# Optimization experiments

Hardware: AMD Instinct MI355X
Metric: run time of the kernel (lower is better)

Reference implementation:

```python
import jax, jax.numpy as jnp
import numpy as np

N, E, D_IN, HEADS, C = 100000, 1600000, 128, 4, 32  # C = out_channels per head


def setup_inputs() -> dict:
    key = jax.random.key(0)
    ks = jax.random.split(key, 10)
    s = 1.0 / np.sqrt(D_IN)
    return {
        "x": jax.random.normal(ks[0], (N, D_IN), jnp.float32),
        "edge_index": jax.random.randint(ks[1], (2, E), 0, N, jnp.int64),
        "Wq": jax.random.normal(ks[2], (D_IN, HEADS * C), jnp.float32) * s,
        "bq": jnp.zeros((HEADS * C,), jnp.float32),
        "Wk": jax.random.normal(ks[3], (D_IN, HEADS * C), jnp.float32) * s,
        "bk": jnp.zeros((HEADS * C,), jnp.float32),
        "Wv": jax.random.normal(ks[4], (D_IN, HEADS * C), jnp.float32) * s,
        "bv": jnp.zeros((HEADS * C,), jnp.float32),
        "Wskip": jax.random.normal(ks[5], (D_IN, HEADS * C), jnp.float32) * s,
        "bskip": jnp.zeros((HEADS * C,), jnp.float32),
    }


def reference(x, edge_index, Wq, bq, Wk, bk, Wv, bv, Wskip, bskip):
    n = x.shape[0]
    src, dst = edge_index[0], edge_index[1]  # message flows src (j) -> dst (i)
    q = (x @ Wq + bq).reshape(n, HEADS, C)
    k = (x @ Wk + bk).reshape(n, HEADS, C)
    v = (x @ Wv + bv).reshape(n, HEADS, C)

    # per-edge attention logits [E, H]
    alpha = jnp.einsum('ehc,ehc->eh', q[dst], k[src]) / jnp.sqrt(jnp.float32(C))

    # segment softmax over incoming edges of each target node
    m = jax.ops.segment_max(alpha, dst, num_segments=n)          # [N, H]
    p = jnp.exp(alpha - m[dst])                                   # [E, H]
    z = jax.ops.segment_sum(p, dst, num_segments=n)               # [N, H]
    w = p / (z[dst] + 1e-16)                                      # [E, H]

    # softmax-weighted scatter aggregation of values
    out = jax.ops.segment_sum(v[src] * w[:, :, None], dst, num_segments=n)
    out = out.reshape(n, HEADS * C)

    # root/skip connection (beta=False default: plain add)
    out = out + x @ Wskip + bskip
    return out
```

## Files before the change

### kernel.cpp

```cpp
#include <hip/hip_runtime.h>

#define DIN 128
#define NHEADS 4
#define CH 32
#define MT 128
#define CHUNK 4096
#define NPB 256
#define EPB_IT 25

typedef _Float16 h8 __attribute__((ext_vector_type(8)));
typedef float f4 __attribute__((ext_vector_type(4)));

__global__ __launch_bounds__(256) void cvt_x(
    const float* __restrict__ x, _Float16* __restrict__ xh, int n4)
{
    int i = blockIdx.x * 256 + threadIdx.x;
    if (i >= n4) return;
    float4 xv = reinterpret_cast<const float4*>(x)[i];
    _Float16 h[4] = {(_Float16)xv.x, (_Float16)xv.y, (_Float16)xv.z, (_Float16)xv.w};
    reinterpret_cast<uint2*>(xh)[i] = *reinterpret_cast<uint2*>(h);
}

__global__ __launch_bounds__(256) void prep_w(
    const float* __restrict__ Wq, const float* __restrict__ Wk,
    const float* __restrict__ Wv, const float* __restrict__ Wsk,
    _Float16* __restrict__ wt)
{
    int i = blockIdx.x * 256 + threadIdx.x;
    if (i >= 4 * 16384) return;
    int mat = i >> 14;
    int rem = i & 16383;
    int n  = rem >> 7;
    int kk = rem & 127;
    const float* W = (mat == 0) ? Wq : (mat == 1) ? Wk : (mat == 2) ? Wv : Wsk;
    wt[i] = (_Float16)W[kk * 128 + n];
}

__global__ __launch_bounds__(256) void qkvs_mfma(
    const _Float16* __restrict__ xh, const _Float16* __restrict__ wt,
    const float* __restrict__ bq, const float* __restrict__ bk,
    const float* __restrict__ bv, const float* __restrict__ bsk,
    _Float16* __restrict__ qh, _Float16* __restrict__ kvh,
    float* __restrict__ outskip, int N)
{
    __shared__ _Float16 As[MT * 128];
    const int t = threadIdx.x;
    const int rowBase = blockIdx.x * MT;
    const int mat = blockIdx.y;

    for (int i = t; i < MT * 16; i += 256) {
        int r  = i >> 4;
        int c8 = i & 15;
        uint4 val = make_uint4(0u, 0u, 0u, 0u);
        int gr = rowBase + r;
        if (gr < N)
            val = reinterpret_cast<const uint4*>(xh)[(size_t)gr * 16 + c8];
        *reinterpret_cast<uint4*>(&As[r * 128 + ((c8 ^ (r & 7)) << 3)]) = val;
    }
    __syncthreads();

    const int wid  = t >> 6;
    const int l    = t & 63;
    const int lm   = l & 15;
    const int quad = l >> 4;

    const _Float16* __restrict__ Bsrc = wt + (size_t)mat * 16384;

    f4 acc[2][8];
    #pragma unroll
    for (int ms = 0; ms < 2; ++ms)
        #pragma unroll
        for (int nt = 0; nt < 8; ++nt)
            acc[ms][nt] = (f4){0.f, 0.f, 0.f, 0.f};

    #pragma unroll
    for (int kq = 0; kq < 4; ++kq) {
        const int c8 = kq * 4 + quad;
        const int k0 = c8 << 3;
        h8 a0 = *reinterpret_cast<const h8*>(
            &As[(wid * 32 + lm) * 128 + ((c8 ^ (lm & 7)) << 3)]);
        h8 a1 = *reinterpret_cast<const h8*>(
            &As[(wid * 32 + 16 + lm) * 128 + ((c8 ^ (lm & 7)) << 3)]);
        #pragma unroll
        for (int nt = 0; nt < 8; ++nt) {
            h8 b = *reinterpret_cast<const h8*>(
                &Bsrc[(size_t)(nt * 16 + lm) * 128 + k0]);
            acc[0][nt] = __builtin_amdgcn_mfma_f32_16x16x32_f16(a0, b, acc[0][nt], 0, 0, 0);
            acc[1][nt] = __builtin_amdgcn_mfma_f32_16x16x32_f16(a1, b, acc[1][nt], 0, 0, 0);
        }
    }

    const float* bias = (mat == 0) ? bq : (mat == 1) ? bk : (mat == 2) ? bv : bsk;

    #pragma unroll
    for (int ms = 0; ms < 2; ++ms) {
        #pragma unroll
        for (int nt = 0; nt < 8; ++nt) {
            int col = nt * 16 + lm;
            float bsv = bias[col];
            #pragma unroll
            for (int i2 = 0; i2 < 4; ++i2) {
                int row = rowBase + wid * 32 + ms * 16 + quad * 4 + i2;
                if (row < N) {
                    float val = acc[ms][nt][i2] + bsv;
                    if (mat == 3)
                        outskip[(size_t)row * 128 + col] = val;
                    else if (mat == 0)
                        qh[(size_t)row * 128 + col] = (_Float16)val;
                    else {
                        size_t off = (size_t)row * 256 + ((col >> 2) << 3)
                                   + (col & 3) + ((mat == 2) ? 4 : 0);
                        kvh[off] = (_Float16)val;
                    }
                }
            }
        }
    }
}

__global__ __launch_bounds__(256) void bucket_hist(
    const int* __restrict__ ei, int* __restrict__ bcnt, int E, int nb)
{
    __shared__ int lds[512];
    for (int b = threadIdx.x; b < nb; b += 256) lds[b] = 0;
    __syncthreads();
    for (long long i = (long long)blockIdx.x * 256 + threadIdx.x; i < E;
         i += (long long)gridDim.x * 256)
        atomicAdd(&lds[ei[(size_t)E + i] >> 8], 1);
    __syncthreads();
    for (int b = threadIdx.x; b < nb; b += 256)
        if (lds[b]) atomicAdd(&bcnt[b], lds[b]);
}

__global__ __launch_bounds__(512) void scan_buckets(
    const int* __restrict__ bcnt, int* __restrict__ boff,
    int* __restrict__ bcur, int nb)
{
    __shared__ int ws[8];
    int t = threadIdx.x, lane = t & 63, wid = t >> 6;
    int v = (t < nb) ? bcnt[t] : 0;
    int s = v;
    #pragma unroll
    for (int off = 1; off < 64; off <<= 1) {
        int n = __shfl_up(s, off);
        if (lane >= off) s += n;
    }
    if (lane == 63) ws[wid] = s;
    __syncthreads();
    int add = 0;
    for (int w = 0; w < wid; ++w) add += ws[w];
    int excl = s - v + add;
    if (t < nb) { boff[t] = excl; bcur[t] = excl; }
    if (t == nb - 1) boff[nb] = excl + v;
}

__global__ __launch_bounds__(256) void bucket_scatter(
    const int* __restrict__ ei, int* __restrict__ bcur,
    uint2* __restrict__ pairs, int E, int nb)
{
    __shared__ int cnt[512];
    int t = threadIdx.x;
    for (int b = t; b < nb; b += 256) cnt[b] = 0;
    __syncthreads();

    long long e0 = (long long)blockIdx.x * (256 * EPB_IT);
    int ps[EPB_IT], pd[EPB_IT];
    #pragma unroll
    for (int j = 0; j < EPB_IT; ++j) {
        long long e = e0 + j * 256 + t;
        if (e < E) {
            ps[j] = ei[e];
            pd[j] = ei[(size_t)E + e];
            atomicAdd(&cnt[pd[j] >> 8], 1);
        } else pd[j] = -1;
    }
    __syncthreads();
    for (int b = t; b < nb; b += 256) {
        int c = cnt[b];
        if (c) cnt[b] = atomicAdd(&bcur[b], c);
    }
    __syncthreads();
    #pragma unroll
    for (int j = 0; j < EPB_IT; ++j) {
        if (pd[j] >= 0) {
            int pos = atomicAdd(&cnt[pd[j] >> 8], 1);
            pairs[pos] = make_uint2((unsigned)ps[j], (unsigned)pd[j]);
        }
    }
}

__global__ __launch_bounds__(256) void bucket_counts(
    const uint2* __restrict__ pairs, const int* __restrict__ boff,
    int* __restrict__ counts, int N)
{
    __shared__ int cnt[NPB];
    int b = blockIdx.x, t = threadIdx.x;
    cnt[t] = 0;
    __syncthreads();
    int s = boff[b], e = boff[b + 1];
    for (int i = s + t; i < e; i += 256)
        atomicAdd(&cnt[pairs[i].y & (NPB - 1)], 1);
    __syncthreads();
    int node = b * NPB + t;
    if (node < N) counts[node] = cnt[t];
}

__global__ __launch_bounds__(256) void chunk_sums(
    const int* __restrict__ counts, int* __restrict__ partials, int N)
{
    int b = blockIdx.x, t = threadIdx.x;
    int base = b * CHUNK + t * 16;
    int s = 0;
    #pragma unroll
    for (int j = 0; j < 16; ++j) {
        int i = base + j;
        if (i < N) s += counts[i];
    }
    #pragma unroll
    for (int off = 1; off < 64; off <<= 1) s += __shfl_xor(s, off);
    __shared__ int ws[4];
    int lane = t & 63, wid = t >> 6;
    if (lane == 0) ws[wid] = s;
    __syncthreads();
    if (t == 0) partials[b] = ws[0] + ws[1] + ws[2] + ws[3];
}

__global__ __launch_bounds__(256) void scan_chunks(
    const int* __restrict__ partials, int* __restrict__ chunkoff, int nch)
{
    __shared__ int ws[4];
    int t = threadIdx.x, lane = t & 63, wid = t >> 6;
    int v = (t < nch) ? partials[t] : 0;
    int s = v;
    #pragma unroll
    for (int off = 1; off < 64; off <<= 1) {
        int n = __shfl_up(s, off);
        if (lane >= off) s += n;
    }
    if (lane == 63) ws[wid] = s;
    __syncthreads();
    int add = 0;
    for (int w = 0; w < wid; ++w) add += ws[w];
    if (t < nch) chunkoff[t] = s - v + add;
}

__global__ __launch_bounds__(256) void scan_write(
    const int* __restrict__ counts, const int* __restrict__ chunkoff,
    int* __restrict__ rowptr, int N)
{
    int b = blockIdx.x, t = threadIdx.x;
    int base = b * CHUNK + t * 16;
    int vals[16];
    int s = 0;
    #pragma unroll
    for (int j = 0; j < 16; ++j) {
        int i = base + j;
        vals[j] = (i < N) ? counts[i] : 0;
        s += vals[j];
    }
    int lane = t & 63, wid = t >> 6;
    int incl = s;
    #pragma unroll
    for (int off = 1; off < 64; off <<= 1) {
        int n = __shfl_up(incl, off);
        if (lane >= off) incl += n;
    }
    __shared__ int ws[4];
    if (lane == 63) ws[wid] = incl;
    __syncthreads();
    int add = chunkoff[b];
    for (int w = 0; w < wid; ++w) add += ws[w];
    int run = incl - s + add;
    #pragma unroll
    for (int j = 0; j < 16; ++j) {
        int i = base + j;
        if (i < N) rowptr[i + 1] = run + vals[j];
        run += vals[j];
    }
    if (b == 0 && t == 0) rowptr[0] = 0;
}

__global__ __launch_bounds__(256) void bucket_place(
    const uint2* __restrict__ pairs, const int* __restrict__ boff,
    const int* __restrict__ rowptr, int* __restrict__ sorted, int N)
{
    __shared__ int cur[NPB];
    int b = blockIdx.x, t = threadIdx.x;
    int node = b * NPB + t;
    cur[t] = (node < N) ? rowptr[node] : 0;
    __syncthreads();
    int s = boff[b], e = boff[b + 1];
    for (int i = s + t; i < e; i += 256) {
        uint2 pr = pairs[i];
        int pos = atomicAdd(&cur[pr.y & (NPB - 1)], 1);
        sorted[pos] = (int)pr.x;
    }
}

__device__ inline float4 cvt4(uint2 r) {
    union { uint2 u; _Float16 h[4]; } c;
    c.u = r;
    return make_float4((float)c.h[0], (float)c.h[1], (float)c.h[2], (float)c.h[3]);
}

__global__ __launch_bounds__(256) void node_aggregate(
    const _Float16* __restrict__ q, const _Float16* __restrict__ kv,
    const int* __restrict__ rowptr, const int* __restrict__ srcs,
    float* __restrict__ out, int N)
{
    int gid  = blockIdx.x * 256 + threadIdx.x;
    int node = gid >> 5;
    if (node >= N) return;
    int l = gid & 31;

    float4 qv = cvt4(reinterpret_cast<const uint2*>(q + (size_t)node * 128)[l]);
    float4 acc = make_float4(0.f, 0.f, 0.f, 0.f);
    float z = 0.f;

    const uint4* kv4 = reinterpret_cast<const uint4*>(kv);
    const float SC = 0.17677669529663687f;
    int e0 = rowptr[node], e1 = rowptr[node + 1];
    int e = e0;
    for (; e + 4 <= e1; e += 4) {
        int s0 = srcs[e], s1 = srcs[e + 1], s2 = srcs[e + 2], s3 = srcs[e + 3];
        uint4 r0 = kv4[(size_t)s0 * 32 + l];
        uint4 r1 = kv4[(size_t)s1 * 32 + l];
        uint4 r2 = kv4[(size_t)s2 * 32 + l];
        uint4 r3 = kv4[(size_t)s3 * 32 + l];
        float4 k0 = cvt4(make_uint2(r0.x, r0.y)), v0 = cvt4(make_uint2(r0.z, r0.w));
        float4 k1 = cvt4(make_uint2(r1.x, r1.y)), v1 = cvt4(make_uint2(r1.z, r1.w));
        float4 k2 = cvt4(make_uint2(r2.x, r2.y)), v2 = cvt4(make_uint2(r2.z, r2.w));
        float4 k3 = cvt4(make_uint2(r3.x, r3.y)), v3 = cvt4(make_uint2(r3.z, r3.w));
        float sa = qv.x * k0.x + qv.y * k0.y + qv.z * k0.z + qv.w * k0.w;
        float sb = qv.x * k1.x + qv.y * k1.y + qv.z * k1.z + qv.w * k1.w;
        float sc = qv.x * k2.x + qv.y * k2.y + qv.z * k2.z + qv.w * k2.w;
        float sd = qv.x * k3.x + qv.y * k3.y + qv.z * k3.z + qv.w * k3.w;
        sa += __shfl_xor(sa, 1); sb += __shfl_xor(sb, 1);
        sc += __shfl_xor(sc, 1); sd += __shfl_xor(sd, 1);
        sa += __shfl_xor(sa, 2); sb += __shfl_xor(sb, 2);
        sc += __shfl_xor(sc, 2); sd += __shfl_xor(sd, 2);
        sa += __shfl_xor(sa, 4); sb += __shfl_xor(sb, 4);
        sc += __shfl_xor(sc, 4); sd += __shfl_xor(sd, 4);
        float pa = __expf(sa * SC), pb = __expf(sb * SC);
        float pc = __expf(sc * SC), pdd = __expf(sd * SC);
        z += (pa + pb) + (pc + pdd);
        acc.x += pa * v0.x + pb * v1.x + pc * v2.x + pdd * v3.x;
        acc.y += pa * v0.y + pb * v1.y + pc * v2.y + pdd * v3.y;
        acc.z += pa * v0.z + pb * v1.z + pc * v2.z + pdd * v3.z;
        acc.w += pa * v0.w + pb * v1.w + pc * v2.w + pdd * v3.w;
    }
    for (; e < e1; ++e) {
        int s0 = srcs[e];
        uint4 r0 = kv4[(size_t)s0 * 32 + l];
        float4 k0 = cvt4(make_uint2(r0.x, r0.y)), v0 = cvt4(make_uint2(r0.z, r0.w));
        float sa = qv.x * k0.x + qv.y * k0.y + qv.z * k0.z + qv.w * k0.w;
        sa += __shfl_xor(sa, 1);
        sa += __shfl_xor(sa, 2);
        sa += __shfl_xor(sa, 4);
        float pa = __expf(sa * SC);
        z += pa;
        acc.x += pa * v0.x; acc.y += pa * v0.y;
        acc.z += pa * v0.z; acc.w += pa * v0.w;
    }

    float inv = 1.f / (z + 1e-16f);
    float4 o = reinterpret_cast<float4*>(out)[(size_t)node * 32 + l];
    o.x += acc.x * inv; o.y += acc.y * inv;
    o.z += acc.z * inv; o.w += acc.w * inv;
    reinterpret_cast<float4*>(out)[(size_t)node * 32 + l] = o;
}

extern "C" void kernel_launch(void* const* d_in, const int* in_sizes, int n_in,
                              void* d_out, int out_size, void* d_ws, size_t ws_size,
                              hipStream_t stream)
{
    const float* x   = (const float*)d_in[0];
    const int*   ei  = (const int*)d_in[1];
    const float* Wq  = (const float*)d_in[2];
    const float* bq  = (const float*)d_in[3];
    const float* Wk  = (const float*)d_in[4];
    const float* bk  = (const float*)d_in[5];
    const float* Wv  = (const float*)d_in[6];
    const float* bv  = (const float*)d_in[7];
    const float* Wsk = (const float*)d_in[8];
    const float* bsk = (const float*)d_in[9];
    float* out = (float*)d_out;

    const int N = in_sizes[0] / DIN;
    const int E = in_sizes[1] / 2;
    const int nb = (N + NPB - 1) / NPB;

    _Float16* xh  = (_Float16*)d_ws;
    _Float16* qh  = xh + (size_t)N * DIN;
    _Float16* kvh = qh + (size_t)N * DIN;
    _Float16* wt  = kvh + (size_t)N * 256;
    uint2* pairs  = (uint2*)(wt + 4 * 16384);
    int* sorted   = (int*)(pairs + (size_t)E);
    int* counts   = sorted + E;
    int* rowptr   = counts + N;
    int* bcnt     = rowptr + (N + 1);
    int* boff     = bcnt + 512;
    int* bcur     = boff + 513;
    int* partials = bcur + 512;
    int* chunkoff = partials + 256;

    hipMemsetAsync(bcnt, 0, 512 * sizeof(int), stream);

    int n4 = N * DIN / 4;
    cvt_x<<<(n4 + 255) / 256, 256, 0, stream>>>(x, xh, n4);
    prep_w<<<(4 * 16384 + 255) / 256, 256, 0, stream>>>(Wq, Wk, Wv, Wsk, wt);

    dim3 ggrid((N + MT - 1) / MT, 4);
    qkvs_mfma<<<ggrid, 256, 0, stream>>>(xh, wt, bq, bk, bv, bsk,
                                         qh, kvh, out, N);

    bucket_hist<<<256, 256, 0, stream>>>(ei, bcnt, E, nb);
    scan_buckets<<<1, 512, 0, stream>>>(bcnt, boff, bcur, nb);
    int sb = (E + 256 * EPB_IT - 1) / (256 * EPB_IT);
    bucket_scatter<<<sb, 256, 0, stream>>>(ei, bcur, pairs, E, nb);
    bucket_counts<<<nb, 256, 0, stream>>>(pairs, boff, counts, N);

    int nch = (N + CHUNK - 1) / CHUNK;
    chunk_sums<<<nch, 256, 0, stream>>>(counts, partials, N);
    scan_chunks<<<1, 256, 0, stream>>>(partials, chunkoff, nch);
    scan_write<<<nch, 256, 0, stream>>>(counts, chunkoff, rowptr, N);

    bucket_place<<<nb, 256, 0, stream>>>(pairs, boff, rowptr, sorted, N);

    int ab = (N * 32 + 255) / 256;
    node_aggregate<<<ab, 256, 0, stream>>>(qh, kvh, rowptr, sorted, out, N);
}
```

Before: 438.3 us.

## Fuse CSR build into persistent grid-synced kernel and convert x inside GEMM

Replaces the chain of small CSR-construction kernels (histogram, scans, scatter, counts, place) plus weight prep with a single persistent 512-block kernel that uses atomic-counter grid barriers between phases. The QKV/skip GEMM now reads fp32 x directly and converts to fp16 while staging into LDS, so the separate conversion kernel and its fp16 copy of x are gone. Each block also loops over all four weight matrices instead of using a 4-wide grid. This removes many launch gaps and one full pass over x, at the cost of spin-wait barriers that only work if all 512 blocks are co-resident, and less GEMM parallelism per launch.

```diff
diff --git a/kernel.cpp b/kernel.cpp
--- a/kernel.cpp
+++ b/kernel.cpp
@@ -7,37 +7,202 @@
 #define CHUNK 4096
 #define NPB 256
 #define EPB_IT 25
+#define CSR_GRID 512
 
 typedef _Float16 h8 __attribute__((ext_vector_type(8)));
 typedef float f4 __attribute__((ext_vector_type(4)));
 
-__global__ __launch_bounds__(256) void cvt_x(
-    const float* __restrict__ x, _Float16* __restrict__ xh, int n4)
-{
-    int i = blockIdx.x * 256 + threadIdx.x;
-    if (i >= n4) return;
-    float4 xv = reinterpret_cast<const float4*>(x)[i];
-    _Float16 h[4] = {(_Float16)xv.x, (_Float16)xv.y, (_Float16)xv.z, (_Float16)xv.w};
-    reinterpret_cast<uint2*>(xh)[i] = *reinterpret_cast<uint2*>(h);
-}
-
-__global__ __launch_bounds__(256) void prep_w(
+__device__ __forceinline__ void gsync(int* bar, int idx, int nblk) {
+    __syncthreads();
+    if (threadIdx.x == 0) {
+        __threadfence();
+        atomicAdd(&bar[idx], 1);
+        while (atomicAdd(&bar[idx], 0) < nblk)
+            __builtin_amdgcn_s_sleep(2);
+    }
+    __syncthreads();
+    __threadfence();
+}
+
+__global__ __launch_bounds__(256, 4) void coop_csr(
     const float* __restrict__ Wq, const float* __restrict__ Wk,
     const float* __restrict__ Wv, const float* __restrict__ Wsk,
-    _Float16* __restrict__ wt)
+    _Float16* __restrict__ wt,
+    const int* __restrict__ ei, uint2* __restrict__ pairs,
+    int* __restrict__ sorted, int* __restrict__ counts,
+    int* __restrict__ rowptr, int* __restrict__ bar, int* __restrict__ bcnt,
+    int* __restrict__ boff, int* __restrict__ bcur,
+    int* __restrict__ partials, int* __restrict__ chunkoff,
+    int E, int N, int nb, int nch)
 {
-    int i = blockIdx.x * 256 + threadIdx.x;
-    if (i >= 4 * 16384) return;
-    int mat = i >> 14;
-    int rem = i & 16383;
-    int n  = rem >> 7;
-    int kk = rem & 127;
-    const float* W = (mat == 0) ? Wq : (mat == 1) ? Wk : (mat == 2) ? Wv : Wsk;
-    wt[i] = (_Float16)W[kk * 128 + n];
+    __shared__ int smem[512];
+    __shared__ int ws[8];
+    const int b = blockIdx.x, t = threadIdx.x;
+    const int nblk = gridDim.x;
+
+    for (int i = b * 256 + t; i < 4 * 16384; i += nblk * 256) {
+        int mat = i >> 14;
+        int rem = i & 16383;
+        int n  = rem >> 7;
+        int kk = rem & 127;
+        const float* W = (mat == 0) ? Wq : (mat == 1) ? Wk : (mat == 2) ? Wv : Wsk;
+        wt[i] = (_Float16)W[kk * 128 + n];
+    }
+    gsync(bar, 0, nblk);
+
+    for (int i = t; i < nb; i += 256) smem[i] = 0;
+    __syncthreads();
+    for (long long i = (long long)b * 256 + t; i < E; i += (long long)nblk * 256)
+        atomicAdd(&smem[ei[(size_t)E + i] >> 8], 1);
+    __syncthreads();
+    for (int i = t; i < nb; i += 256)
+        if (smem[i]) atomicAdd(&bcnt[i], smem[i]);
+    gsync(bar, 1, nblk);
+
+    if (b == 0) {
+        int i0 = 2 * t, i1 = 2 * t + 1;
+        int a = (i0 < nb) ? bcnt[i0] : 0;
+        int c = (i1 < nb) ? bcnt[i1] : 0;
+        int s = a + c;
+        int lane = t & 63, wid = t >> 6;
+        int incl = s;
+        #pragma unroll
+        for (int off = 1; off < 64; off <<= 1) {
+            int n = __shfl_up(incl, off);
+            if (lane >= off) incl += n;
+        }
+        if (lane == 63) ws[wid] = incl;
+        __syncthreads();
+        int add = 0;
+        for (int w = 0; w < wid; ++w) add += ws[w];
+        int excl = incl - s + add;
+        if (i0 < nb) { boff[i0] = excl;     bcur[i0] = excl; }
+        if (i1 < nb) { boff[i1] = excl + a; bcur[i1] = excl + a; }
+        if (t == 255) boff[nb] = excl + s;
+    }
+    gsync(bar, 2, nblk);
+
+    for (long long c0 = (long long)b * (256 * EPB_IT); c0 < E;
+         c0 += (long long)nblk * (256 * EPB_IT)) {
+        for (int i = t; i < nb; i += 256) smem[i] = 0;
+        __syncthreads();
+        int ps[EPB_IT], pd[EPB_IT];
+        #pragma unroll
+        for (int j = 0; j < EPB_IT; ++j) {
+            long long e = c0 + j * 256 + t;
+            if (e < E) {
+                ps[j] = ei[e];
+                pd[j] = ei[(size_t)E + e];
+                atomicAdd(&smem[pd[j] >> 8], 1);
+            } else pd[j] = -1;
+        }
+        __syncthreads();
+        for (int i = t; i < nb; i += 256) {
+            int c = smem[i];
+            if (c) smem[i] = atomicAdd(&bcur[i], c);
+        }
+        __syncthreads();
+        #pragma unroll
+        for (int j = 0; j < EPB_IT; ++j) {
+            if (pd[j] >= 0) {
+                int pos = atomicAdd(&smem[pd[j] >> 8], 1);
+                pairs[pos] = make_uint2((unsigned)ps[j], (unsigned)pd[j]);
+            }
+        }
+        __syncthreads();
+    }
+    gsync(bar, 3, nblk);
+
+    for (int bb = b; bb < nb; bb += nblk) {
+        smem[t] = 0;
+        __syncthreads();
+        int s = boff[bb], e = boff[bb + 1];
+        for (int i = s + t; i < e; i += 256)
+            atomicAdd(&smem[pairs[i].y & (NPB - 1)], 1);
+        __syncthreads();
+        int node = bb * NPB + t;
+        if (node < N) counts[node] = smem[t];
+        __syncthreads();
+    }
+    gsync(bar, 4, nblk);
+
+    if (b < nch) {
+        int base = b * CHUNK + t * 16;
+        int s = 0;
+        #pragma unroll
+        for (int j = 0; j < 16; ++j) {
+            int i = base + j;
+            if (i < N) s += counts[i];
+        }
+        #pragma unroll
+        for (int off = 1; off < 64; off <<= 1) s += __shfl_xor(s, off);
+        int lane = t & 63, wid = t >> 6;
+        if (lane == 0) ws[wid] = s;
+        __syncthreads();
+        if (t == 0) partials[b] = ws[0] + ws[1] + ws[2] + ws[3];
+    }
+    gsync(bar, 5, nblk);
+
+    if (b == 0 && t < 64) {
+        int v = (t < nch) ? partials[t] : 0;
+        int s = v;
+        #pragma unroll
+        for (int off = 1; off < 64; off <<= 1) {
+            int n = __shfl_up(s, off);
+            if (t >= off) s += n;
+        }
+        if (t < nch) chunkoff[t] = s - v;
+    }
+    gsync(bar, 6, nblk);
+
+    if (b < nch) {
+        int base = b * CHUNK + t * 16;
+        int vals[16];
+        int s = 0;
+        #pragma unroll
+        for (int j = 0; j < 16; ++j) {
+            int i = base + j;
+            vals[j] = (i < N) ? counts[i] : 0;
+            s += vals[j];
+        }
+        int lane = t & 63, wid = t >> 6;
+        int incl = s;
+        #pragma unroll
+        for (int off = 1; off < 64; off <<= 1) {
+            int n = __shfl_up(incl, off);
+            if (lane >= off) incl += n;
+        }
+        if (lane == 63) ws[wid] = incl;
+        __syncthreads();
+        int add = chunkoff[b];
+        for (int w = 0; w < wid; ++w) add += ws[w];
+        int run = incl - s + add;
+        #pragma unroll
+        for (int j = 0; j < 16; ++j) {
+            int i = base + j;
+            if (i < N) rowptr[i + 1] = run + vals[j];
+            run += vals[j];
+        }
+        if (b == 0 && t == 0) rowptr[0] = 0;
+    }
+    gsync(bar, 7, nblk);
+
+    for (int bb = b; bb < nb; bb += nblk) {
+        int node = bb * NPB + t;
+        smem[t] = (node < N) ? rowptr[node] : 0;
+        __syncthreads();
+        int s = boff[bb], e = boff[bb + 1];
+        for (int i = s + t; i < e; i += 256) {
+            uint2 pr = pairs[i];
+            int pos = atomicAdd(&smem[pr.y & (NPB - 1)], 1);
+            sorted[pos] = (int)pr.x;
+        }
+        __syncthreads();
+    }
 }
 
 __global__ __launch_bounds__(256) void qkvs_mfma(
-    const _Float16* __restrict__ xh, const _Float16* __restrict__ wt,
+    const float* __restrict__ x, const _Float16* __restrict__ wt,
     const float* __restrict__ bq, const float* __restrict__ bk,
     const float* __restrict__ bv, const float* __restrict__ bsk,
     _Float16* __restrict__ qh, _Float16* __restrict__ kvh,
@@ -46,16 +211,22 @@
     __shared__ _Float16 As[MT * 128];
     const int t = threadIdx.x;
     const int rowBase = blockIdx.x * MT;
-    const int mat = blockIdx.y;
-
+
+    const float4* x4 = reinterpret_cast<const float4*>(x);
     for (int i = t; i < MT * 16; i += 256) {
         int r  = i >> 4;
         int c8 = i & 15;
-        uint4 val = make_uint4(0u, 0u, 0u, 0u);
+        h8 hv = {};
         int gr = rowBase + r;
-        if (gr < N)
-            val = reinterpret_cast<const uint4*>(xh)[(size_t)gr * 16 + c8];
-        *reinterpret_cast<uint4*>(&As[r * 128 + ((c8 ^ (r & 7)) << 3)]) = val;
+        if (gr < N) {
+            float4 f0 = x4[(size_t)gr * 32 + c8 * 2];
+            float4 f1 = x4[(size_t)gr * 32 + c8 * 2 + 1];
+            hv[0] = (_Float16)f0.x; hv[1] = (_Float16)f0.y;
+            hv[2] = (_Float16)f0.z; hv[3] = (_Float16)f0.w;
+            hv[4] = (_Float16)f1.x; hv[5] = (_Float16)f1.y;
+            hv[6] = (_Float16)f1.z; hv[7] = (_Float16)f1.w;
+        }
+        *reinterpret_cast<h8*>(&As[r * 128 + ((c8 ^ (r & 7)) << 3)]) = hv;
     }
     __syncthreads();
 
@@ -64,236 +235,59 @@
     const int lm   = l & 15;
     const int quad = l >> 4;
 
-    const _Float16* __restrict__ Bsrc = wt + (size_t)mat * 16384;
-
-    f4 acc[2][8];
-    #pragma unroll
-    for (int ms = 0; ms < 2; ++ms)
-        #pragma unroll
-        for (int nt = 0; nt < 8; ++nt)
-            acc[ms][nt] = (f4){0.f, 0.f, 0.f, 0.f};
-
-    #pragma unroll
-    for (int kq = 0; kq < 4; ++kq) {
-        const int c8 = kq * 4 + quad;
-        const int k0 = c8 << 3;
-        h8 a0 = *reinterpret_cast<const h8*>(
-            &As[(wid * 32 + lm) * 128 + ((c8 ^ (lm & 7)) << 3)]);
-        h8 a1 = *reinterpret_cast<const h8*>(
-            &As[(wid * 32 + 16 + lm) * 128 + ((c8 ^ (lm & 7)) << 3)]);
-        #pragma unroll
-        for (int nt = 0; nt < 8; ++nt) {
-            h8 b = *reinterpret_cast<const h8*>(
-                &Bsrc[(size_t)(nt * 16 + lm) * 128 + k0]);
-            acc[0][nt] = __builtin_amdgcn_mfma_f32_16x16x32_f16(a0, b, acc[0][nt], 0, 0, 0);
-            acc[1][nt] = __builtin_amdgcn_mfma_f32_16x16x32_f16(a1, b, acc[1][nt], 0, 0, 0);
-        }
-    }
-
-    const float* bias = (mat == 0) ? bq : (mat == 1) ? bk : (mat == 2) ? bv : bsk;
-
-    #pragma unroll
-    for (int ms = 0; ms < 2; ++ms) {
-        #pragma unroll
-        for (int nt = 0; nt < 8; ++nt) {
-            int col = nt * 16 + lm;
-            float bsv = bias[col];
+    for (int mat = 0; mat < 4; ++mat) {
+        const _Float16* __restrict__ Bsrc = wt + (size_t)mat * 16384;
+
+        f4 acc[2][8];
+        #pragma unroll
+        for (int ms = 0; ms < 2; ++ms)
             #pragma unroll
-            for (int i2 = 0; i2 < 4; ++i2) {
-                int row = rowBase + wid * 32 + ms * 16 + quad * 4 + i2;
-                if (row < N) {
-                    float val = acc[ms][nt][i2] + bsv;
-                    if (mat == 3)
-                        outskip[(size_t)row * 128 + col] = val;
-                    else if (mat == 0)
-                        qh[(size_t)row * 128 + col] = (_Float16)val;
-                    else {
-                        size_t off = (size_t)row * 256 + ((col >> 2) << 3)
-                                   + (col & 3) + ((mat == 2) ? 4 : 0);
-                        kvh[off] = (_Float16)val;
+            for (int nt = 0; nt < 8; ++nt)
+                acc[ms][nt] = (f4){0.f, 0.f, 0.f, 0.f};
+
+        #pragma unroll
+        for (int kq = 0; kq < 4; ++kq) {
+            const int c8 = kq * 4 + quad;
+            const int k0 = c8 << 3;
+            h8 a0 = *reinterpret_cast<const h8*>(
+                &As[(wid * 32 + lm) * 128 + ((c8 ^ (lm & 7)) << 3)]);
+            h8 a1 = *reinterpret_cast<const h8*>(
+                &As[(wid * 32 + 16 + lm) * 128 + ((c8 ^ (lm & 7)) << 3)]);
+            #pragma unroll
+            for (int nt = 0; nt < 8; ++nt) {
+                h8 bfr = *reinterpret_cast<const h8*>(
+                    &Bsrc[(size_t)(nt * 16 + lm) * 128 + k0]);
+                acc[0][nt] = __builtin_amdgcn_mfma_f32_16x16x32_f16(a0, bfr, acc[0][nt], 0, 0, 0);
+                acc[1][nt] = __builtin_amdgcn_mfma_f32_16x16x32_f16(a1, bfr, acc[1][nt], 0, 0, 0);
+            }
+        }
+
+        const float* bias = (mat == 0) ? bq : (mat == 1) ? bk : (mat == 2) ? bv : bsk;
+
+        #pragma unroll
+        for (int ms = 0; ms < 2; ++ms) {
+            #pragma unroll
+            for (int nt = 0; nt < 8; ++nt) {
+                int col = nt * 16 + lm;
+                float bsv = bias[col];
+                #pragma unroll
+                for (int i2 = 0; i2 < 4; ++i2) {
+                    int row = rowBase + wid * 32 + ms * 16 + quad * 4 + i2;
+                    if (row < N) {
+                        float val = acc[ms][nt][i2] + bsv;
+                        if (mat == 3)
+                            outskip[(size_t)row * 128 + col] = val;
+                        else if (mat == 0)
+                            qh[(size_t)row * 128 + col] = (_Float16)val;
+                        else {
+                            size_t off = (size_t)row * 256 + ((col >> 2) << 3)
+                                       + (col & 3) + ((mat == 2) ? 4 : 0);
+                            kvh[off] = (_Float16)val;
+                        }
                     }
                 }
             }
         }
-    }
-}
-
-__global__ __launch_bounds__(256) void bucket_hist(
-    const int* __restrict__ ei, int* __restrict__ bcnt, int E, int nb)
-{
-    __shared__ int lds[512];
-    for (int b = threadIdx.x; b < nb; b += 256) lds[b] = 0;
-    __syncthreads();
-    for (long long i = (long long)blockIdx.x * 256 + threadIdx.x; i < E;
-         i += (long long)gridDim.x * 256)
-        atomicAdd(&lds[ei[(size_t)E + i] >> 8], 1);
-    __syncthreads();
-    for (int b = threadIdx.x; b < nb; b += 256)
-        if (lds[b]) atomicAdd(&bcnt[b], lds[b]);
-}
-
-__global__ __launch_bounds__(512) void scan_buckets(
-    const int* __restrict__ bcnt, int* __restrict__ boff,
-    int* __restrict__ bcur, int nb)
-{
-    __shared__ int ws[8];
-    int t = threadIdx.x, lane = t & 63, wid = t >> 6;
-    int v = (t < nb) ? bcnt[t] : 0;
-    int s = v;
-    #pragma unroll
-    for (int off = 1; off < 64; off <<= 1) {
-        int n = __shfl_up(s, off);
-        if (lane >= off) s += n;
-    }
-    if (lane == 63) ws[wid] = s;
-    __syncthreads();
-    int add = 0;
-    for (int w = 0; w < wid; ++w) add += ws[w];
-    int excl = s - v + add;
-    if (t < nb) { boff[t] = excl; bcur[t] = excl; }
-    if (t == nb - 1) boff[nb] = excl + v;
-}
-
-__global__ __launch_bounds__(256) void bucket_scatter(
-    const int* __restrict__ ei, int* __restrict__ bcur,
-    uint2* __restrict__ pairs, int E, int nb)
-{
-    __shared__ int cnt[512];
-    int t = threadIdx.x;
-    for (int b = t; b < nb; b += 256) cnt[b] = 0;
-    __syncthreads();
-
-    long long e0 = (long long)blockIdx.x * (256 * EPB_IT);
-    int ps[EPB_IT], pd[EPB_IT];
-    #pragma unroll
-    for (int j = 0; j < EPB_IT; ++j) {
-        long long e = e0 + j * 256 + t;
-        if (e < E) {
-            ps[j] = ei[e];
-            pd[j] = ei[(size_t)E + e];
-            atomicAdd(&cnt[pd[j] >> 8], 1);
-        } else pd[j] = -1;
-    }
-    __syncthreads();
-    for (int b = t; b < nb; b += 256) {
-        int c = cnt[b];
-        if (c) cnt[b] = atomicAdd(&bcur[b], c);
-    }
-    __syncthreads();
-    #pragma unroll
-    for (int j = 0; j < EPB_IT; ++j) {
-        if (pd[j] >= 0) {
-            int pos = atomicAdd(&cnt[pd[j] >> 8], 1);
-            pairs[pos] = make_uint2((unsigned)ps[j], (unsigned)pd[j]);
-        }
-    }
-}
-
-__global__ __launch_bounds__(256) void bucket_counts(
-    const uint2* __restrict__ pairs, const int* __restrict__ boff,
-    int* __restrict__ counts, int N)
-{
-    __shared__ int cnt[NPB];
-    int b = blockIdx.x, t = threadIdx.x;
-    cnt[t] = 0;
-    __syncthreads();
-    int s = boff[b], e = boff[b + 1];
-    for (int i = s + t; i < e; i += 256)
-        atomicAdd(&cnt[pairs[i].y & (NPB - 1)], 1);
-    __syncthreads();
-    int node = b * NPB + t;
-    if (node < N) counts[node] = cnt[t];
-}
-
-__global__ __launch_bounds__(256) void chunk_sums(
-    const int* __restrict__ counts, int* __restrict__ partials, int N)
-{
-    int b = blockIdx.x, t = threadIdx.x;
-    int base = b * CHUNK + t * 16;
-    int s = 0;
-    #pragma unroll
-    for (int j = 0; j < 16; ++j) {
-        int i = base + j;
-        if (i < N) s += counts[i];
-    }
-    #pragma unroll
-    for (int off = 1; off < 64; off <<= 1) s += __shfl_xor(s, off);
-    __shared__ int ws[4];
-    int lane = t & 63, wid = t >> 6;
-    if (lane == 0) ws[wid] = s;
-    __syncthreads();
-    if (t == 0) partials[b] = ws[0] + ws[1] + ws[2] + ws[3];
-}
-
-__global__ __launch_bounds__(256) void scan_chunks(
-    const int* __restrict__ partials, int* __restrict__ chunkoff, int nch)
-{
-    __shared__ int ws[4];
-    int t = threadIdx.x, lane = t & 63, wid = t >> 6;
-    int v = (t < nch) ? partials[t] : 0;
-    int s = v;
-    #pragma unroll
-    for (int off = 1; off < 64; off <<= 1) {
-        int n = __shfl_up(s, off);
-        if (lane >= off) s += n;
-    }
-    if (lane == 63) ws[wid] = s;
-    __syncthreads();
-    int add = 0;
-    for (int w = 0; w < wid; ++w) add += ws[w];
-    if (t < nch) chunkoff[t] = s - v + add;
-}
-
-__global__ __launch_bounds__(256) void scan_write(
-    const int* __restrict__ counts, const int* __restrict__ chunkoff,
-    int* __restrict__ rowptr, int N)
-{
-    int b = blockIdx.x, t = threadIdx.x;
-    int base = b * CHUNK + t * 16;
-    int vals[16];
-    int s = 0;
-    #pragma unroll
-    for (int j = 0; j < 16; ++j) {
-        int i = base + j;
-        vals[j] = (i < N) ? counts[i] : 0;
-        s += vals[j];
-    }
-    int lane = t & 63, wid = t >> 6;
-    int incl = s;
-    #pragma unroll
-    for (int off = 1; off < 64; off <<= 1) {
-        int n = __shfl_up(incl, off);
-        if (lane >= off) incl += n;
-    }
-    __shared__ int ws[4];
-    if (lane == 63) ws[wid] = incl;
-    __syncthreads();
-    int add = chunkoff[b];
-    for (int w = 0; w < wid; ++w) add += ws[w];
-    int run = incl - s + add;
-    #pragma unroll
-    for (int j = 0; j < 16; ++j) {
-        int i = base + j;
-        if (i < N) rowptr[i + 1] = run + vals[j];
-        run += vals[j];
-    }
-    if (b == 0 && t == 0) rowptr[0] = 0;
-}
-
-__global__ __launch_bounds__(256) void bucket_place(
-    const uint2* __restrict__ pairs, const int* __restrict__ boff,
-    const int* __restrict__ rowptr, int* __restrict__ sorted, int N)
-{
-    __shared__ int cur[NPB];
-    int b = blockIdx.x, t = threadIdx.x;
-    int node = b * NPB + t;
-    cur[t] = (node < N) ? rowptr[node] : 0;
-    __syncthreads();
-    int s = boff[b], e = boff[b + 1];
-    for (int i = s + t; i < e; i += 256) {
-        uint2 pr = pairs[i];
-        int pos = atomicAdd(&cur[pr.y & (NPB - 1)], 1);
-        sorted[pos] = (int)pr.x;
     }
 }
 
@@ -389,43 +383,30 @@
     const int N = in_sizes[0] / DIN;
     const int E = in_sizes[1] / 2;
     const int nb = (N + NPB - 1) / NPB;
-
-    _Float16* xh  = (_Float16*)d_ws;
-    _Float16* qh  = xh + (size_t)N * DIN;
+    const int nch = (N + CHUNK - 1) / CHUNK;
+
+    _Float16* qh  = (_Float16*)d_ws;
     _Float16* kvh = qh + (size_t)N * DIN;
     _Float16* wt  = kvh + (size_t)N * 256;
     uint2* pairs  = (uint2*)(wt + 4 * 16384);
     int* sorted   = (int*)(pairs + (size_t)E);
     int* counts   = sorted + E;
     int* rowptr   = counts + N;
-    int* bcnt     = rowptr + (N + 1);
+    int* bar      = rowptr + (N + 1);
+    int* bcnt     = bar + 8;
     int* boff     = bcnt + 512;
     int* bcur     = boff + 513;
     int* partials = bcur + 512;
     int* chunkoff = partials + 256;
 
-    hipMemsetAsync(bcnt, 0, 512 * sizeof(int), stream);
-
-    int n4 = N * DIN / 4;
-    cvt_x<<<(n4 + 255) / 256, 256, 0, stream>>>(x, xh, n4);
-    prep_w<<<(4 * 16384 + 255) / 256, 256, 0, stream>>>(Wq, Wk, Wv, Wsk, wt);
-
-    dim3 ggrid((N + MT - 1) / MT, 4);
-    qkvs_mfma<<<ggrid, 256, 0, stream>>>(xh, wt, bq, bk, bv, bsk,
-                                         qh, kvh, out, N);
-
-    bucket_hist<<<256, 256, 0, stream>>>(ei, bcnt, E, nb);
-    scan_buckets<<<1, 512, 0, stream>>>(bcnt, boff, bcur, nb);
-    int sb = (E + 256 * EPB_IT - 1) / (256 * EPB_IT);
-    bucket_scatter<<<sb, 256, 0, stream>>>(ei, bcur, pairs, E, nb);
-    bucket_counts<<<nb, 256, 0, stream>>>(pairs, boff, counts, N);
-
-    int nch = (N + CHUNK - 1) / CHUNK;
-    chunk_sums<<<nch, 256, 0, stream>>>(counts, partials, N);
-    scan_chunks<<<1, 256, 0, stream>>>(partials, chunkoff, nch);
-    scan_write<<<nch, 256, 0, stream>>>(counts, chunkoff, rowptr, N);
-
-    bucket_place<<<nb, 256, 0, stream>>>(pairs, boff, rowptr, sorted, N);
+    hipMemsetAsync(bar, 0, 520 * sizeof(int), stream);
+
+    coop_csr<<<CSR_GRID, 256, 0, stream>>>(
+        Wq, Wk, Wv, Wsk, wt, ei, pairs, sorted, counts, rowptr,
+        bar, bcnt, boff, bcur, partials, chunkoff, E, N, nb, nch);
+
+    qkvs_mfma<<<(N + MT - 1) / MT, 256, 0, stream>>>(
+        x, wt, bq, bk, bv, bsk, qh, kvh, out, N);
 
     int ab = (N * 32 + 255) / 256;
     node_aggregate<<<ab, 256, 0, stream>>>(qh, kvh, rowptr, sorted, out, N);
```

Result: slower. 953.4 us (+117.6%).

## Fuse input conversion into QKV GEMM and collapse CSR build into one kernel

Applied to the files above, without the earlier changes.

Removes the separate x and weight fp16 conversion kernels: the GEMM now loads fp32 x and converts it into shared memory, loops over all four weight matrices per block, and reads the fp32 weights directly with strided per-element loads. Separately, the per-node count, chunk scan and placement kernels are merged into a single per-bucket kernel that scans counts locally, offsetting by the bucket base, because each bucket covers a contiguous node range. This saves several launches and the xh round trip, but the B-fragment loads become uncoalesced strided global reads with inline conversion, which may slow the GEMM.

```diff
diff --git a/kernel.cpp b/kernel.cpp
--- a/kernel.cpp
+++ b/kernel.cpp
@@ -4,58 +4,41 @@
 #define NHEADS 4
 #define CH 32
 #define MT 128
-#define CHUNK 4096
 #define NPB 256
 #define EPB_IT 25
 
 typedef _Float16 h8 __attribute__((ext_vector_type(8)));
 typedef float f4 __attribute__((ext_vector_type(4)));
 
-__global__ __launch_bounds__(256) void cvt_x(
-    const float* __restrict__ x, _Float16* __restrict__ xh, int n4)
-{
-    int i = blockIdx.x * 256 + threadIdx.x;
-    if (i >= n4) return;
-    float4 xv = reinterpret_cast<const float4*>(x)[i];
-    _Float16 h[4] = {(_Float16)xv.x, (_Float16)xv.y, (_Float16)xv.z, (_Float16)xv.w};
-    reinterpret_cast<uint2*>(xh)[i] = *reinterpret_cast<uint2*>(h);
-}
-
-__global__ __launch_bounds__(256) void prep_w(
-    const float* __restrict__ Wq, const float* __restrict__ Wk,
-    const float* __restrict__ Wv, const float* __restrict__ Wsk,
-    _Float16* __restrict__ wt)
-{
-    int i = blockIdx.x * 256 + threadIdx.x;
-    if (i >= 4 * 16384) return;
-    int mat = i >> 14;
-    int rem = i & 16383;
-    int n  = rem >> 7;
-    int kk = rem & 127;
-    const float* W = (mat == 0) ? Wq : (mat == 1) ? Wk : (mat == 2) ? Wv : Wsk;
-    wt[i] = (_Float16)W[kk * 128 + n];
-}
-
 __global__ __launch_bounds__(256) void qkvs_mfma(
-    const _Float16* __restrict__ xh, const _Float16* __restrict__ wt,
+    const float* __restrict__ x, const float* __restrict__ Wq,
+    const float* __restrict__ Wk, const float* __restrict__ Wv,
+    const float* __restrict__ Wsk,
     const float* __restrict__ bq, const float* __restrict__ bk,
     const float* __restrict__ bv, const float* __restrict__ bsk,
+    _Float16* __restrict__ wt,
     _Float16* __restrict__ qh, _Float16* __restrict__ kvh,
     float* __restrict__ outskip, int N)
 {
     __shared__ _Float16 As[MT * 128];
     const int t = threadIdx.x;
     const int rowBase = blockIdx.x * MT;
-    const int mat = blockIdx.y;
-
+
+    const float4* x4 = reinterpret_cast<const float4*>(x);
     for (int i = t; i < MT * 16; i += 256) {
         int r  = i >> 4;
         int c8 = i & 15;
-        uint4 val = make_uint4(0u, 0u, 0u, 0u);
+        h8 hv = {};
         int gr = rowBase + r;
-        if (gr < N)
-            val = reinterpret_cast<const uint4*>(xh)[(size_t)gr * 16 + c8];
-        *reinterpret_cast<uint4*>(&As[r * 128 + ((c8 ^ (r & 7)) << 3)]) = val;
+        if (gr < N) {
+            float4 f0 = x4[(size_t)gr * 32 + c8 * 2];
+            float4 f1 = x4[(size_t)gr * 32 + c8 * 2 + 1];
+            hv[0] = (_Float16)f0.x; hv[1] = (_Float16)f0.y;
+            hv[2] = (_Float16)f0.z; hv[3] = (_Float16)f0.w;
+            hv[4] = (_Float16)f1.x; hv[5] = (_Float16)f1.y;
+            hv[6] = (_Float16)f1.z; hv[7] = (_Float16)f1.w;
+        }
+        *reinterpret_cast<h8*>(&As[r * 128 + ((c8 ^ (r & 7)) << 3)]) = hv;
     }
     __syncthreads();
 
@@ -64,53 +47,61 @@
     const int lm   = l & 15;
     const int quad = l >> 4;
 
-    const _Float16* __restrict__ Bsrc = wt + (size_t)mat * 16384;
-
-    f4 acc[2][8];
-    #pragma unroll
-    for (int ms = 0; ms < 2; ++ms)
+    const float* Wm[4] = {Wq, Wk, Wv, Wsk};
+    const float* bm[4] = {bq, bk, bv, bsk};
+
+    for (int mat = 0; mat < 4; ++mat) {
+        const float* __restrict__ W = Wm[mat];
+
+        f4 acc[2][8];
         #pragma unroll
-        for (int nt = 0; nt < 8; ++nt)
-            acc[ms][nt] = (f4){0.f, 0.f, 0.f, 0.f};
-
-    #pragma unroll
-    for (int kq = 0; kq < 4; ++kq) {
-        const int c8 = kq * 4 + quad;
-        const int k0 = c8 << 3;
-        h8 a0 = *reinterpret_cast<const h8*>(
-            &As[(wid * 32 + lm) * 128 + ((c8 ^ (lm & 7)) << 3)]);
-        h8 a1 = *reinterpret_cast<const h8*>(
-            &As[(wid * 32 + 16 + lm) * 128 + ((c8 ^ (lm & 7)) << 3)]);
+        for (int ms = 0; ms < 2; ++ms)
+            #pragma unroll
+            for (int nt = 0; nt < 8; ++nt)
+                acc[ms][nt] = (f4){0.f, 0.f, 0.f, 0.f};
+
         #pragma unroll
-        for (int nt = 0; nt < 8; ++nt) {
-            h8 b = *reinterpret_cast<const h8*>(
-                &Bsrc[(size_t)(nt * 16 + lm) * 128 + k0]);
-            acc[0][nt] = __builtin_amdgcn_mfma_f32_16x16x32_f16(a0, b, acc[0][nt], 0, 0, 0);
-            acc[1][nt] = __builtin_amdgcn_mfma_f32_16x16x32_f16(a1, b, acc[1][nt], 0, 0, 0);
+        for (int kq = 0; kq < 4; ++kq) {
+            const int c8 = kq * 4 + quad;
+            const int k0 = c8 << 3;
+            h8 a0 = *reinterpret_cast<const h8*>(
+                &As[(wid * 32 + lm) * 128 + ((c8 ^ (lm & 7)) << 3)]);
+            h8 a1 = *reinterpret_cast<const h8*>(
+                &As[(wid * 32 + 16 + lm) * 128 + ((c8 ^ (lm & 7)) << 3)]);
+            #pragma unroll
+            for (int nt = 0; nt < 8; ++nt) {
+                int col = nt * 16 + lm;
+                h8 bfr;
+                #pragma unroll
+                for (int j = 0; j < 8; ++j)
+                    bfr[j] = (_Float16)W[(size_t)(k0 + j) * 128 + col];
+                acc[0][nt] = __builtin_amdgcn_mfma_f32_16x16x32_f16(a0, bfr, acc[0][nt], 0, 0, 0);
+                acc[1][nt] = __builtin_amdgcn_mfma_f32_16x16x32_f16(a1, bfr, acc[1][nt], 0, 0, 0);
+            }
         }
-    }
-
-    const float* bias = (mat == 0) ? bq : (mat == 1) ? bk : (mat == 2) ? bv : bsk;
-
-    #pragma unroll
-    for (int ms = 0; ms < 2; ++ms) {
+
+        const float* bias = bm[mat];
+
         #pragma unroll
-        for (int nt = 0; nt < 8; ++nt) {
-            int col = nt * 16 + lm;
-            float bsv = bias[col];
+        for (int ms = 0; ms < 2; ++ms) {
             #pragma unroll
-            for (int i2 = 0; i2 < 4; ++i2) {
-                int row = rowBase + wid * 32 + ms * 16 + quad * 4 + i2;
-                if (row < N) {
-                    float val = acc[ms][nt][i2] + bsv;
-                    if (mat == 3)
-                        outskip[(size_t)row * 128 + col] = val;
-                    else if (mat == 0)
-                        qh[(size_t)row * 128 + col] = (_Float16)val;
-                    else {
-                        size_t off = (size_t)row * 256 + ((col >> 2) << 3)
-                                   + (col & 3) + ((mat == 2) ? 4 : 0);
-                        kvh[off] = (_Float16)val;
+            for (int nt = 0; nt < 8; ++nt) {
+                int col = nt * 16 + lm;
+                float bsv = bias[col];
+                #pragma unroll
+                for (int i2 = 0; i2 < 4; ++i2) {
+                    int row = rowBase + wid * 32 + ms * 16 + quad * 4 + i2;
+                    if (row < N) {
+                        float val = acc[ms][nt][i2] + bsv;
+                        if (mat == 3)
+                            outskip[(size_t)row * 128 + col] = val;
+                        else if (mat == 0)
+                            qh[(size_t)row * 128 + col] = (_Float16)val;
+                        else {
+                            size_t off = (size_t)row * 256 + ((col >> 2) << 3)
+                                       + (col & 3) + ((mat == 2) ? 4 : 0);
+                            kvh[off] = (_Float16)val;
+                        }
                     }
                 }
             }
@@ -189,11 +180,12 @@
     }
 }
 
-__global__ __launch_bounds__(256) void bucket_counts(
+__global__ __launch_bounds__(256) void bucket_csr(
     const uint2* __restrict__ pairs, const int* __restrict__ boff,
-    int* __restrict__ counts, int N)
+    int* __restrict__ rowptr, int* __restrict__ sorted, int N, int E, int nb)
 {
     __shared__ int cnt[NPB];
+    __shared__ int ws[4];
     int b = blockIdx.x, t = threadIdx.x;
     cnt[t] = 0;
     __syncthreads();
@@ -201,98 +193,30 @@
     for (int i = s + t; i < e; i += 256)
         atomicAdd(&cnt[pairs[i].y & (NPB - 1)], 1);
     __syncthreads();
-    int node = b * NPB + t;
-    if (node < N) counts[node] = cnt[t];
-}
-
-__global__ __launch_bounds__(256) void chunk_sums(
-    const int* __restrict__ counts, int* __restrict__ partials, int N)
-{
-    int b = blockIdx.x, t = threadIdx.x;
-    int base = b * CHUNK + t * 16;
-    int s = 0;
-    #pragma unroll
-    for (int j = 0; j < 16; ++j) {
-        int i = base + j;
-        if (i < N) s += counts[i];
-    }
-    #pragma unroll
-    for (int off = 1; off < 64; off <<= 1) s += __shfl_xor(s, off);
-    __shared__ int ws[4];
+
+    int v = cnt[t];
     int lane = t & 63, wid = t >> 6;
-    if (lane == 0) ws[wid] = s;
-    __syncthreads();
-    if (t == 0) partials[b] = ws[0] + ws[1] + ws[2] + ws[3];
-}
-
-__global__ __launch_bounds__(256) void scan_chunks(
-    const int* __restrict__ partials, int* __restrict__ chunkoff, int nch)
-{
-    __shared__ int ws[4];
-    int t = threadIdx.x, lane = t & 63, wid = t >> 6;
-    int v = (t < nch) ? partials[t] : 0;
-    int s = v;
-    #pragma unroll
-    for (int off = 1; off < 64; off <<= 1) {
-        int n = __shfl_up(s, off);
-        if (lane >= off) s += n;
-    }
-    if (lane == 63) ws[wid] = s;
-    __syncthreads();
-    int add = 0;
-    for (int w = 0; w < wid; ++w) add += ws[w];
-    if (t < nch) chunkoff[t] = s - v + add;
-}
-
-__global__ __launch_bounds__(256) void scan_write(
-    const int* __restrict__ counts, const int* __restrict__ chunkoff,
-    int* __restrict__ rowptr, int N)
-{
-    int b = blockIdx.x, t = threadIdx.x;
-    int base = b * CHUNK + t * 16;
-    int vals[16];
-    int s = 0;
-    #pragma unroll
-    for (int j = 0; j < 16; ++j) {
-        int i = base + j;
-        vals[j] = (i < N) ? counts[i] : 0;
-        s += vals[j];
-    }
-    int lane = t & 63, wid = t >> 6;
-    int incl = s;
+    int incl = v;
     #pragma unroll
     for (int off = 1; off < 64; off <<= 1) {
         int n = __shfl_up(incl, off);
         if (lane >= off) incl += n;
     }
-    __shared__ int ws[4];
     if (lane == 63) ws[wid] = incl;
     __syncthreads();
-    int add = chunkoff[b];
+    int add = boff[b];
     for (int w = 0; w < wid; ++w) add += ws[w];
-    int run = incl - s + add;
-    #pragma unroll
-    for (int j = 0; j < 16; ++j) {
-        int i = base + j;
-        if (i < N) rowptr[i + 1] = run + vals[j];
-        run += vals[j];
-    }
-    if (b == 0 && t == 0) rowptr[0] = 0;
-}
-
-__global__ __launch_bounds__(256) void bucket_place(
-    const uint2* __restrict__ pairs, const int* __restrict__ boff,
-    const int* __restrict__ rowptr, int* __restrict__ sorted, int N)
-{
-    __shared__ int cur[NPB];
-    int b = blockIdx.x, t = threadIdx.x;
+    int excl = incl - v + add;
+
     int node = b * NPB + t;
-    cur[t] = (node < N) ? rowptr[node] : 0;
-    __syncthreads();
-    int s = boff[b], e = boff[b + 1];
+    if (node < N) rowptr[node] = excl;
+    if (b == 0 && t == 0) rowptr[N] = E;
+
+    cnt[t] = excl;
+    __syncthreads();
     for (int i = s + t; i < e; i += 256) {
         uint2 pr = pairs[i];
-        int pos = atomicAdd(&cur[pr.y & (NPB - 1)], 1);
+        int pos = atomicAdd(&cnt[pr.y & (NPB - 1)], 1);
         sorted[pos] = (int)pr.x;
     }
 }
@@ -390,42 +314,26 @@
     const int E = in_sizes[1] / 2;
     const int nb = (N + NPB - 1) / NPB;
 
-    _Float16* xh  = (_Float16*)d_ws;
-    _Float16* qh  = xh + (size_t)N * DIN;
+    _Float16* qh  = (_Float16*)d_ws;
     _Float16* kvh = qh + (size_t)N * DIN;
     _Float16* wt  = kvh + (size_t)N * 256;
     uint2* pairs  = (uint2*)(wt + 4 * 16384);
     int* sorted   = (int*)(pairs + (size_t)E);
-    int* counts   = sorted + E;
-    int* rowptr   = counts + N;
+    int* rowptr   = sorted + E;
     int* bcnt     = rowptr + (N + 1);
     int* boff     = bcnt + 512;
     int* bcur     = boff + 513;
-    int* partials = bcur + 512;
-    int* chunkoff = partials + 256;
 
     hipMemsetAsync(bcnt, 0, 512 * sizeof(int), stream);
 
-    int n4 = N * DIN / 4;
-    cvt_x<<<(n4 + 255) / 256, 256, 0, stream>>>(x, xh, n4);
-    prep_w<<<(4 * 16384 + 255) / 256, 256, 0, stream>>>(Wq, Wk, Wv, Wsk, wt);
-
-    dim3 ggrid((N + MT - 1) / MT, 4);
-    qkvs_mfma<<<ggrid, 256, 0, stream>>>(xh, wt, bq, bk, bv, bsk,
-                                         qh, kvh, out, N);
+    qkvs_mfma<<<(N + MT - 1) / MT, 256, 0, stream>>>(
+        x, Wq, Wk, Wv, Wsk, bq, bk, bv, bsk, wt, qh, kvh, out, N);
 
     bucket_hist<<<256, 256, 0, stream>>>(ei, bcnt, E, nb);
     scan_buckets<<<1, 512, 0, stream>>>(bcnt, boff, bcur, nb);
     int sb = (E + 256 * EPB_IT - 1) / (256 * EPB_IT);
     bucket_scatter<<<sb, 256, 0, stream>>>(ei, bcur, pairs, E, nb);
-    bucket_counts<<<nb, 256, 0, stream>>>(pairs, boff, counts, N);
-
-    int nch = (N + CHUNK - 1) / CHUNK;
-    chunk_sums<<<nch, 256, 0, stream>>>(counts, partials, N);
-    scan_chunks<<<1, 256, 0, stream>>>(partials, chunkoff, nch);
-    scan_write<<<nch, 256, 0, stream>>>(counts, chunkoff, rowptr, N);
-
-    bucket_place<<<nb, 256, 0, stream>>>(pairs, boff, rowptr, sorted, N);
+    bucket_csr<<<nb, 256, 0, stream>>>(pairs, boff, rowptr, sorted, N, E, nb);
 
     int ab = (N * 32 + 255) / 256;
     node_aggregate<<<ab, 256, 0, stream>>>(qh, kvh, rowptr, sorted, out, N);
```

New measurement: 526.4 us. 1.2x slower.
